# Kernel optimization log

Hardware: AMD Instinct MI355X
Metric: run time of the kernel (lower is better)

The kernel has to match this reference:

```python
import jax, jax.numpy as jnp
import numpy as np

N_CLASSES = 16384
M = 2
D = 128


def setup_inputs() -> dict:
    key = jax.random.key(0)
    k1, k2 = jax.random.split(key)
    x = jax.random.normal(k1, (N_CLASSES * M, D), dtype=jnp.float32)
    anchor_idx = jax.random.randint(k2, (N_CLASSES,), 0, M, dtype=jnp.int64 if jax.config.jax_enable_x64 else jnp.int32).astype(jnp.int32)
    pos_idx = (1 - anchor_idx).astype(jnp.int32)  # randperm(2) -> positive is the other sample
    return {"x": x, "anchor_idx": anchor_idx, "pos_idx": pos_idx}


def reference(x, anchor_idx, pos_idx):
    # x: [N*M, D]; anchor_idx/pos_idx: [N] in [0, M)
    N = anchor_idx.shape[0]
    Dx = x.shape[1]
    xr = x.reshape(N, M, Dx)
    anchors = jnp.take_along_axis(xr, anchor_idx[:, None, None], axis=1)[:, 0, :]    # [N, D]
    positives = jnp.take_along_axis(xr, pos_idx[:, None, None], axis=1)[:, 0, :]     # [N, D]
    negs = xr[:, 1, :]                                                               # [N, D] (sample 1 of every class)
    # score[i, j] = a_i . (neg_j - pos_i) = a_i . neg_j - a_i . pos_i
    S = anchors @ negs.T                                                             # [N, N]
    ap = jnp.sum(anchors * positives, axis=1)                                        # [N]
    logits = S - ap[:, None]
    mask = ~jnp.eye(N, dtype=bool)                                                   # exclude j == i (own class)
    sums = jnp.sum(jnp.where(mask, jnp.exp(logits), jnp.float32(0.0)), axis=1)       # [N]
    return jnp.sum(jnp.log1p(sums))
```

## Files before the change

### kernel.cpp

```cpp
#include <hip/hip_runtime.h>
#include <hip/hip_bf16.h>
#include <math.h>

#define N_CLS 16384
#define DDIM  128
#define LOG2E 1.4426950408889634f

#if __has_builtin(__builtin_amdgcn_exp2f)
#define EXP2(x) __builtin_amdgcn_exp2f(x)
#else
#define EXP2(x) exp2f(x)
#endif

typedef __attribute__((ext_vector_type(8))) short short8;
typedef __attribute__((ext_vector_type(16))) float f32x16;

__device__ __forceinline__ unsigned short f2bf(float f) {
    __hip_bfloat16 h = __float2bfloat16(f);
    return *(unsigned short*)&h;
}

__global__ __launch_bounds__(256)
void prep_kernel(const float* __restrict__ x,
                 const int* __restrict__ aidx,
                 float* __restrict__ ap,
                 unsigned short* __restrict__ Afrag,
                 unsigned short* __restrict__ Bfrag,
                 float* __restrict__ out) {
    const int u  = blockIdx.x * 256 + threadIdx.x;
    const int i  = u >> 4;
    const int sl = u & 15;
    const int k0 = sl * 8;

    const float* pa = x + (2L * i) * DDIM + k0;
    float fa[8], fb[8];
    *(float4*)&fa[0] = *(const float4*)(pa);
    *(float4*)&fa[4] = *(const float4*)(pa + 4);
    *(float4*)&fb[0] = *(const float4*)(pa + DDIM);
    *(float4*)&fb[4] = *(const float4*)(pa + DDIM + 4);
    const bool sel = (aidx[i] != 0);

    short8 A, B;
    float d = 0.0f;
    #pragma unroll
    for (int j = 0; j < 8; ++j) {
        const float av = sel ? fb[j] : fa[j];
        A[j] = (short)f2bf(av * LOG2E);
        B[j] = (short)f2bf(fb[j]);
        d += fa[j] * fb[j];
    }
    const long dst = (long)(i >> 5) * 4096 + (sl >> 1) * 512 +
                     ((sl & 1) * 32 + (i & 31)) * 8;
    *(short8*)(Afrag + dst) = A;
    *(short8*)(Bfrag + dst) = B;

    d += __shfl_xor(d, 1, 64);
    d += __shfl_xor(d, 2, 64);
    d += __shfl_xor(d, 4, 64);
    d += __shfl_xor(d, 8, 64);
    if (sl == 0) ap[i] = d;
    if (u == 0) out[0] = 0.0f;
}

__global__ __launch_bounds__(256, 3)
void fused_kernel(const unsigned short* __restrict__ Afrag,
                  const unsigned short* __restrict__ Bfrag,
                  float* __restrict__ partial) {
    __shared__ __align__(16) unsigned short bs[2][4096];
    const int tid  = threadIdx.x;
    const int lane = tid & 63;
    const int w    = tid >> 6;
    const int l31  = lane & 31;
    const int hi   = lane >> 5;
    const int cg   = blockIdx.x & 15;
    const int rt   = blockIdx.x >> 4;
    const int r0   = rt * 8 + w * 2;
    const int r1   = r0 + 1;

    short8 af0[8], af1[8];
    {
        const unsigned short* a0 = Afrag + (long)r0 * 4096 + lane * 8;
        const unsigned short* a1 = Afrag + (long)r1 * 4096 + lane * 8;
        #pragma unroll
        for (int kc = 0; kc < 8; ++kc) {
            af0[kc] = *(const short8*)(a0 + kc * 512);
            af1[kc] = *(const short8*)(a1 + kc * 512);
        }
    }
    const unsigned short* bbase = Bfrag + (long)cg * (32L * 4096) + lane * 8;
    const int wchunk = w * 1024;

    int ctd0 = r0 - cg * 32;
    int ctd1 = r1 - cg * 32;
    if (ctd0 < 0 || ctd0 >= 32) ctd0 = -1000;
    if (ctd1 < 0 || ctd1 >= 32) ctd1 = -1000;

    float rs0[16], rs1[16];
    #pragma unroll
    for (int q = 0; q < 16; ++q) { rs0[q] = 0.0f; rs1[q] = 0.0f; }

    {
        short8 s0 = *(const short8*)(bbase + wchunk);
        short8 s1 = *(const short8*)(bbase + wchunk + 512);
        *(short8*)(&bs[0][wchunk + lane * 8]) = s0;
        *(short8*)(&bs[0][wchunk + 512 + lane * 8]) = s1;
    }
    __syncthreads();

    for (int ct = 0; ct < 32; ++ct) {
        const int cur = ct & 1;
        const long nt = (ct < 31) ? (long)(ct + 1) : 31L;
        short8 n0 = *(const short8*)(bbase + nt * 4096 + wchunk);
        short8 n1 = *(const short8*)(bbase + nt * 4096 + wchunk + 512);

        f32x16 acc0, acc1;
        #pragma unroll
        for (int q = 0; q < 16; ++q) { acc0[q] = 0.0f; acc1[q] = 0.0f; }

        const unsigned short* bp = &bs[cur][lane * 8];
        __builtin_amdgcn_s_setprio(1);
        #pragma unroll
        for (int kc = 0; kc < 8; ++kc) {
            short8 b = *(const short8*)(bp + kc * 512);
            acc0 = __builtin_amdgcn_mfma_f32_32x32x16_bf16(af0[kc], b, acc0, 0, 0, 0);
            acc1 = __builtin_amdgcn_mfma_f32_32x32x16_bf16(af1[kc], b, acc1, 0, 0, 0);
        }
        __builtin_amdgcn_s_setprio(0);

        if (ct == ctd0) {
            #pragma unroll
            for (int q = 0; q < 16; ++q) {
                const float e = EXP2(acc0[q]);
                const int row = (q & 3) + 8 * (q >> 2) + 4 * hi;
                rs0[q] += (l31 == row) ? 0.0f : e;
            }
        } else {
            #pragma unroll
            for (int q = 0; q < 16; ++q) rs0[q] += EXP2(acc0[q]);
        }
        if (ct == ctd1) {
            #pragma unroll
            for (int q = 0; q < 16; ++q) {
                const float e = EXP2(acc1[q]);
                const int row = (q & 3) + 8 * (q >> 2) + 4 * hi;
                rs1[q] += (l31 == row) ? 0.0f : e;
            }
        } else {
            #pragma unroll
            for (int q = 0; q < 16; ++q) rs1[q] += EXP2(acc1[q]);
        }

        *(short8*)(&bs[cur ^ 1][wchunk + lane * 8]) = n0;
        *(short8*)(&bs[cur ^ 1][wchunk + 512 + lane * 8]) = n1;
        __syncthreads();
    }

    #pragma unroll
    for (int q = 0; q < 16; ++q) {
        float v0 = rs0[q], v1 = rs1[q];
        v0 += __shfl_xor(v0, 1, 64);  v1 += __shfl_xor(v1, 1, 64);
        v0 += __shfl_xor(v0, 2, 64);  v1 += __shfl_xor(v1, 2, 64);
        v0 += __shfl_xor(v0, 4, 64);  v1 += __shfl_xor(v1, 4, 64);
        v0 += __shfl_xor(v0, 8, 64);  v1 += __shfl_xor(v1, 8, 64);
        v0 += __shfl_xor(v0, 16, 64); v1 += __shfl_xor(v1, 16, 64);
        if (l31 == 0) {
            const int row = (q & 3) + 8 * (q >> 2) + 4 * hi;
            partial[(long)cg * N_CLS + (long)r0 * 32 + row] = v0;
            partial[(long)cg * N_CLS + (long)r1 * 32 + row] = v1;
        }
    }
}

__global__ __launch_bounds__(256)
void finalize_kernel(const float* __restrict__ partial,
                     const float* __restrict__ ap,
                     float* __restrict__ out) {
    __shared__ float red[256];
    const int t = threadIdx.x;
    const int row = blockIdx.x * 256 + t;
    float s = 0.0f;
    #pragma unroll
    for (int p = 0; p < 16; ++p) s += partial[(long)p * N_CLS + row];
    const float u = logf(s) - ap[row];
    const float loss = (u > 25.0f) ? u : log1pf(__expf(u));
    red[t] = loss;
    __syncthreads();
    for (int st = 128; st > 0; st >>= 1) {
        if (t < st) red[t] += red[t + st];
        __syncthreads();
    }
    if (t == 0) atomicAdd(out, red[0]);
}

extern "C" void kernel_launch(void* const* d_in, const int* in_sizes, int n_in,
                              void* d_out, int out_size, void* d_ws, size_t ws_size,
                              hipStream_t stream) {
    const float* x    = (const float*)d_in[0];
    const int*   aidx = (const int*)d_in[1];

    char* ws = (char*)d_ws;
    float* ap             = (float*)(ws);
    float* partial        = (float*)(ws + 131072);
    unsigned short* Afrag = (unsigned short*)(ws + 131072 + 1048576);
    unsigned short* Bfrag = (unsigned short*)(ws + 131072 + 1048576 + 4194304);

    prep_kernel<<<1024, 256, 0, stream>>>(x, aidx, ap, Afrag, Bfrag, (float*)d_out);
    fused_kernel<<<1024, 256, 0, stream>>>(Afrag, Bfrag, partial);
    finalize_kernel<<<64, 256, 0, stream>>>(partial, ap, (float*)d_out);
}
```

Before: 144.8 us.

## Load B fragments directly into registers with double-buffered prefetch, dropping LDS staging

Removes the shared-memory double buffer and per-tile __syncthreads; each wave now loads full B fragment tiles straight from global memory into two register buffers, prefetching the next tile while computing the current one. Accumulator zeroing is folded into the first MFMA. Occupancy hint lowered from 3 to 2 blocks to make room for the extra registers. Each wave now reads all of B independently (4x more global/L2 traffic per block) in exchange for no LDS round-trip or barriers.

```diff
diff --git a/kernel.cpp b/kernel.cpp
--- a/kernel.cpp
+++ b/kernel.cpp
@@ -62,19 +62,18 @@
     if (u == 0) out[0] = 0.0f;
 }
 
-__global__ __launch_bounds__(256, 3)
+__global__ __launch_bounds__(256, 2)
 void fused_kernel(const unsigned short* __restrict__ Afrag,
                   const unsigned short* __restrict__ Bfrag,
                   float* __restrict__ partial) {
-    __shared__ __align__(16) unsigned short bs[2][4096];
     const int tid  = threadIdx.x;
     const int lane = tid & 63;
     const int w    = tid >> 6;
     const int l31  = lane & 31;
     const int hi   = lane >> 5;
     const int cg   = blockIdx.x & 15;
-    const int rt   = blockIdx.x >> 4;
-    const int r0   = rt * 8 + w * 2;
+    const int rg   = blockIdx.x >> 4;
+    const int r0   = rg * 8 + w * 2;
     const int r1   = r0 + 1;
 
     short8 af0[8], af1[8];
@@ -87,8 +86,7 @@
             af1[kc] = *(const short8*)(a1 + kc * 512);
         }
     }
-    const unsigned short* bbase = Bfrag + (long)cg * (32L * 4096) + lane * 8;
-    const int wchunk = w * 1024;
+    const unsigned short* bbase = Bfrag + (long)(cg * 32) * 4096 + lane * 8;
 
     int ctd0 = r0 - cg * 32;
     int ctd1 = r1 - cg * 32;
@@ -99,34 +97,21 @@
     #pragma unroll
     for (int q = 0; q < 16; ++q) { rs0[q] = 0.0f; rs1[q] = 0.0f; }
 
-    {
-        short8 s0 = *(const short8*)(bbase + wchunk);
-        short8 s1 = *(const short8*)(bbase + wchunk + 512);
-        *(short8*)(&bs[0][wchunk + lane * 8]) = s0;
-        *(short8*)(&bs[0][wchunk + 512 + lane * 8]) = s1;
-    }
-    __syncthreads();
-
-    for (int ct = 0; ct < 32; ++ct) {
-        const int cur = ct & 1;
-        const long nt = (ct < 31) ? (long)(ct + 1) : 31L;
-        short8 n0 = *(const short8*)(bbase + nt * 4096 + wchunk);
-        short8 n1 = *(const short8*)(bbase + nt * 4096 + wchunk + 512);
-
+    const f32x16 zacc = {0.0f, 0.0f, 0.0f, 0.0f, 0.0f, 0.0f, 0.0f, 0.0f,
+                         0.0f, 0.0f, 0.0f, 0.0f, 0.0f, 0.0f, 0.0f, 0.0f};
+    short8 bP[8], bQ[8];
+
+    auto compute_epi = [&](short8 (&bk)[8], int ct) {
         f32x16 acc0, acc1;
-        #pragma unroll
-        for (int q = 0; q < 16; ++q) { acc0[q] = 0.0f; acc1[q] = 0.0f; }
-
-        const unsigned short* bp = &bs[cur][lane * 8];
         __builtin_amdgcn_s_setprio(1);
         #pragma unroll
         for (int kc = 0; kc < 8; ++kc) {
-            short8 b = *(const short8*)(bp + kc * 512);
-            acc0 = __builtin_amdgcn_mfma_f32_32x32x16_bf16(af0[kc], b, acc0, 0, 0, 0);
-            acc1 = __builtin_amdgcn_mfma_f32_32x32x16_bf16(af1[kc], b, acc1, 0, 0, 0);
+            acc0 = __builtin_amdgcn_mfma_f32_32x32x16_bf16(
+                       af0[kc], bk[kc], (kc == 0) ? zacc : acc0, 0, 0, 0);
+            acc1 = __builtin_amdgcn_mfma_f32_32x32x16_bf16(
+                       af1[kc], bk[kc], (kc == 0) ? zacc : acc1, 0, 0, 0);
         }
         __builtin_amdgcn_s_setprio(0);
-
         if (ct == ctd0) {
             #pragma unroll
             for (int q = 0; q < 16; ++q) {
@@ -149,10 +134,24 @@
             #pragma unroll
             for (int q = 0; q < 16; ++q) rs1[q] += EXP2(acc1[q]);
         }
-
-        *(short8*)(&bs[cur ^ 1][wchunk + lane * 8]) = n0;
-        *(short8*)(&bs[cur ^ 1][wchunk + 512 + lane * 8]) = n1;
-        __syncthreads();
+    };
+
+    #pragma unroll
+    for (int kc = 0; kc < 8; ++kc)
+        bP[kc] = *(const short8*)(bbase + kc * 512);
+
+    for (int ct = 0; ct < 32; ct += 2) {
+        const unsigned short* p1 = bbase + (long)(ct + 1) * 4096;
+        #pragma unroll
+        for (int kc = 0; kc < 8; ++kc)
+            bQ[kc] = *(const short8*)(p1 + kc * 512);
+        compute_epi(bP, ct);
+
+        const unsigned short* p2 = bbase + (long)((ct < 30) ? ct + 2 : 31) * 4096;
+        #pragma unroll
+        for (int kc = 0; kc < 8; ++kc)
+            bP[kc] = *(const short8*)(p2 + kc * 512);
+        compute_epi(bQ, ct + 1);
     }
 
     #pragma unroll
```

New measurement: 144.5 us. Within noise of the previous version (-0.2%).
